# Kernel optimization log

Measured on AMD Instinct MI355X. Metric: run time of the kernel, lower is better.

## Reference

```python
import jax, jax.numpy as jnp
import numpy as np

N_NODES = 100000
N_EDGES = 3200000
F_IN = 16
F_HID = 32


def _gcn_conv(x, row, col, edge_w, W, b, num_nodes):
    # PyG GCNConv: gcn_norm with add_self_loops=True (fill_value=1.0),
    # symmetric normalization, then x @ W.T aggregated over edges, + bias.
    loop = jnp.arange(num_nodes)
    r = jnp.concatenate([row, loop])
    c = jnp.concatenate([col, loop])
    ew = jnp.concatenate([edge_w, jnp.ones((num_nodes,), dtype=edge_w.dtype)])
    deg = jax.ops.segment_sum(ew, c, num_segments=num_nodes)
    dis = jnp.where(deg > 0, jax.lax.rsqrt(deg), 0.0)
    norm = dis[r] * ew * dis[c]  # [E+N]
    xw = x @ W.T                 # [N, out]
    msg = xw[r] * norm[:, None]  # gather + scale
    out = jax.ops.segment_sum(msg, c, num_segments=num_nodes)
    return out + b


def setup_inputs() -> dict:
    key = jax.random.key(0)
    ks = jax.random.split(key, 8)
    x = jax.random.normal(ks[0], (N_NODES, F_IN), dtype=jnp.float32)
    edge_index = jax.random.randint(ks[1], (2, N_EDGES), 0, N_NODES, dtype=jnp.int64)
    edge_w = jax.random.uniform(ks[2], (N_EDGES,), dtype=jnp.float32)
    W1 = jax.random.normal(ks[3], (F_HID, F_IN), dtype=jnp.float32) * 0.1
    b1 = jax.random.normal(ks[4], (F_HID,), dtype=jnp.float32) * 0.1
    W2 = jax.random.normal(ks[5], (F_IN, F_HID), dtype=jnp.float32) * 0.1
    b2 = jax.random.normal(ks[6], (F_IN,), dtype=jnp.float32) * 0.1
    return {"x": x, "edge_index": edge_index, "edge_w": edge_w,
            "W1": W1, "b1": b1, "W2": W2, "b2": b2, "num_nodes": N_NODES}


def reference(x, edge_index, edge_w, W1, b1, W2, b2, num_nodes):
    row, col = edge_index[0], edge_index[1]
    h = _gcn_conv(x, row, col, edge_w, W1, b1, num_nodes)
    h = jax.nn.relu(h)
    out = _gcn_conv(h, row, col, edge_w, W2, b2, num_nodes)
    return out
```

## Files before the change

### kernel.cpp

```cpp
#include <hip/hip_runtime.h>
#include <hip/hip_fp16.h>
#include <cstdint>


#define BS 256
#define CHUNKS 256
#define NST 1024

__device__ __forceinline__ int2 nt_load_edge(const int2* p) {
    long long v = __builtin_nontemporal_load((const long long*)p);
    int2 r;
    r.x = (int)(v & 0xFFFFFFFFll);
    r.y = (int)(v >> 32);
    return r;
}

__device__ __forceinline__ float4 load_h4(const __half* p) {
    uint2 u = *(const uint2*)p;
    __half2 p0 = *(__half2*)&u.x;
    __half2 p1 = *(__half2*)&u.y;
    float2 f0 = __half22float2(p0);
    float2 f1 = __half22float2(p1);
    float4 r;
    r.x = f0.x; r.y = f0.y; r.z = f1.x; r.w = f1.y;
    return r;
}

__global__ __launch_bounds__(1024) void hist_kernel(
        const int* __restrict__ col, int* __restrict__ part,
        int E, int nbuck, int per) {
    extern __shared__ int sh[];
    for (int t = threadIdx.x; t < nbuck; t += blockDim.x) sh[t] = 0;
    __syncthreads();
    int lo = blockIdx.x * per, hi = min(E, lo + per);
    for (int e = lo + threadIdx.x; e < hi; e += blockDim.x)
        atomicAdd(&sh[col[e] >> 8], 1);
    __syncthreads();
    for (int t = threadIdx.x; t < nbuck; t += blockDim.x)
        part[(size_t)blockIdx.x * nbuck + t] = sh[t];
}

__global__ void colscan_kernel(const int* __restrict__ part, int* __restrict__ base,
                               int* __restrict__ tot, int nbuck) {
    int b = blockIdx.x;
    if (b >= nbuck) return;
    int lane = threadIdx.x;
    int off = 0;
    for (int g = 0; g < CHUNKS; g += 64) {
        int c = g + lane;
        int v = part[(size_t)c * nbuck + b];
        int s = v;
        #pragma unroll
        for (int d = 1; d < 64; d <<= 1) {
            int t = __shfl_up(s, d);
            if (lane >= d) s += t;
        }
        base[(size_t)c * nbuck + b] = off + (s - v);
        off += __shfl(s, 63);
    }
    if (lane == 0) tot[b] = off;
}

__global__ void bscan_kernel(const int* __restrict__ tot, int* __restrict__ start,
                             int nbuck, int E) {
    __shared__ int s[512];
    int tid = threadIdx.x;
    int v = (tid < nbuck) ? tot[tid] : 0;
    s[tid] = v;
    __syncthreads();
    for (int off = 1; off < 512; off <<= 1) {
        int t = (tid >= off) ? s[tid - off] : 0;
        __syncthreads();
        s[tid] += t;
        __syncthreads();
    }
    if (tid < nbuck) start[tid] = s[tid] - v;
    if (tid == 0) start[nbuck] = E;
}

__global__ __launch_bounds__(1024) void place_kernel(
        const int* __restrict__ row, const int* __restrict__ col,
        const float* __restrict__ ew,
        const int* __restrict__ start, const int* __restrict__ base,
        int2* __restrict__ rw, int E, int nbuck, int per) {
    extern __shared__ int sh[];
    int* lbase = sh;
    int* cnt2  = sh + nbuck;
    int c = blockIdx.x;
    for (int t = threadIdx.x; t < nbuck; t += blockDim.x) {
        lbase[t] = start[t] + base[(size_t)c * nbuck + t];
        cnt2[t] = 0;
    }
    __syncthreads();
    int lo = c * per, hi = min(E, lo + per);
    const int stride = blockDim.x;
    int e = lo + threadIdx.x;
    for (; e + 3 * stride < hi; e += 4 * stride) {
        int cc[4], rr[4];
        float w[4];
#pragma unroll
        for (int k = 0; k < 4; ++k) {
            cc[k] = col[e + k * stride];
            rr[k] = row[e + k * stride];
            w[k]  = ew[e + k * stride];
        }
        int p[4];
#pragma unroll
        for (int k = 0; k < 4; ++k) {
            int b = cc[k] >> 8;
            p[k] = lbase[b] + atomicAdd(&cnt2[b], 1);
        }
#pragma unroll
        for (int k = 0; k < 4; ++k) {
            int2 v;
            v.x = rr[k] | ((cc[k] & 255) << 20);
            v.y = __float_as_int(w[k]);
            rw[p[k]] = v;
        }
    }
    for (; e < hi; e += stride) {
        int cc = col[e];
        int b = cc >> 8;
        int p = lbase[b] + atomicAdd(&cnt2[b], 1);
        int2 v;
        v.x = row[e] | ((cc & 255) << 20);
        v.y = __float_as_int(ew[e]);
        rw[p] = v;
    }
}

__global__ __launch_bounds__(NST) void nodesort_kernel(
        const int2* __restrict__ rw, const int* __restrict__ start,
        int2* __restrict__ rw2, int* __restrict__ ptr,
        float* __restrict__ dis, int N, int E, int nbuck) {
    __shared__ int cnt[BS];
    __shared__ float fdeg[BS];
    __shared__ int fill[BS];
    __shared__ int stmp[BS];
    int b = blockIdx.x, tid = threadIdx.x;
    if (tid < BS) { cnt[tid] = 0; fdeg[tid] = 0.f; }
    __syncthreads();
    int s0 = start[b], s1 = start[b + 1];

    {
        int e = s0 + tid;
        for (; e + 3 * NST < s1; e += 4 * NST) {
            int2 v[4];
#pragma unroll
            for (int k = 0; k < 4; ++k) v[k] = rw[e + k * NST];
#pragma unroll
            for (int k = 0; k < 4; ++k) {
                int cl = v[k].x >> 20;
                atomicAdd(&cnt[cl], 1);
                atomicAdd(&fdeg[cl], __int_as_float(v[k].y));
            }
        }
        for (; e < s1; e += NST) {
            int2 v = rw[e];
            int cl = v.x >> 20;
            atomicAdd(&cnt[cl], 1);
            atomicAdd(&fdeg[cl], __int_as_float(v.y));
        }
    }
    __syncthreads();

    int myc = 0;
    if (tid < BS) { myc = cnt[tid]; stmp[tid] = myc; }
    __syncthreads();
    for (int off = 1; off < BS; off <<= 1) {
        int t = 0;
        if (tid < BS && tid >= off) t = stmp[tid - off];
        __syncthreads();
        if (tid < BS) stmp[tid] += t;
        __syncthreads();
    }
    if (tid < BS) {
        int excl = stmp[tid] - myc;
        ptr[b * BS + tid] = s0 + excl;
        fill[tid] = excl;
        int node = b * BS + tid;
        if (node < N) dis[node] = rsqrtf(fdeg[tid] + 1.0f);
    }
    __syncthreads();

    {
        int e = s0 + tid;
        for (; e + 3 * NST < s1; e += 4 * NST) {
            int2 v[4];
#pragma unroll
            for (int k = 0; k < 4; ++k) v[k] = rw[e + k * NST];
            int p[4];
#pragma unroll
            for (int k = 0; k < 4; ++k)
                p[k] = s0 + atomicAdd(&fill[v[k].x >> 20], 1);
#pragma unroll
            for (int k = 0; k < 4; ++k) {
                int2 o;
                o.x = (v[k].x & 0xFFFFF) << 5;
                o.y = v[k].y;
                rw2[p[k]] = o;
            }
        }
        for (; e < s1; e += NST) {
            int2 v = rw[e];
            int p = s0 + atomicAdd(&fill[v.x >> 20], 1);
            int2 o;
            o.x = (v.x & 0xFFFFF) << 5;
            o.y = v.y;
            rw2[p] = o;
        }
    }
    if (b == 0 && tid == 0) ptr[nbuck * BS] = E;
}

__global__ void xsc_kernel(const float* __restrict__ x, const float* __restrict__ dis,
                           __half* __restrict__ xsc, int N) {
    int i = blockIdx.x * 256 + threadIdx.x;
    if (i >= N) return;
    float d = dis[i];
    const float4* xr = (const float4*)(x + (size_t)i * 16);
    __half2 h[8];
#pragma unroll
    for (int k = 0; k < 4; ++k) {
        float4 v = xr[k];
        h[2*k]   = __floats2half2_rn(v.x * d, v.y * d);
        h[2*k+1] = __floats2half2_rn(v.z * d, v.w * d);
    }
    uint4* dst = (uint4*)(xsc + (size_t)i * 16);
    dst[0] = *(uint4*)&h[0];
    dst[1] = *(uint4*)&h[4];
}

template <int FINAL>
__global__ __launch_bounds__(256) void gather_kernel(
        const int* __restrict__ ptr, const int2* __restrict__ rw2,
        const __half* __restrict__ src, const float* __restrict__ dis,
        const float* __restrict__ b2, float* __restrict__ dst, int N) {
    int tid  = threadIdx.x;
    int wave = tid >> 6;
    int lane = tid & 63;
    int g = lane >> 4;
    int s = (lane >> 2) & 3;
    int q = lane & 3;
    int node = (blockIdx.x * 4 + wave) * 4 + g;
    if (node >= N) return;
    int s0 = ptr[node], s1 = ptr[node + 1];

    const char* srcb = (const char*)src;
    float4 a0 = {0.f, 0.f, 0.f, 0.f}, a1 = {0.f, 0.f, 0.f, 0.f};
    int e = s0 + s;
    for (; e + 4 < s1; e += 8) {
        int2 v0 = nt_load_edge(&rw2[e]);
        int2 v1 = nt_load_edge(&rw2[e + 4]);
        float4 x0 = load_h4((const __half*)(srcb + v0.x) + q * 4);
        float4 x1 = load_h4((const __half*)(srcb + v1.x) + q * 4);
        float w0 = __int_as_float(v0.y), w1 = __int_as_float(v1.y);
        a0.x += w0 * x0.x; a0.y += w0 * x0.y; a0.z += w0 * x0.z; a0.w += w0 * x0.w;
        a1.x += w1 * x1.x; a1.y += w1 * x1.y; a1.z += w1 * x1.z; a1.w += w1 * x1.w;
    }
    if (e < s1) {
        int2 v0 = nt_load_edge(&rw2[e]);
        float4 x0 = load_h4((const __half*)(srcb + v0.x) + q * 4);
        float w0 = __int_as_float(v0.y);
        a0.x += w0 * x0.x; a0.y += w0 * x0.y; a0.z += w0 * x0.z; a0.w += w0 * x0.w;
    }
    a0.x += a1.x; a0.y += a1.y; a0.z += a1.z; a0.w += a1.w;
#pragma unroll
    for (int m = 4; m <= 8; m <<= 1) {
        a0.x += __shfl_xor(a0.x, m);
        a0.y += __shfl_xor(a0.y, m);
        a0.z += __shfl_xor(a0.z, m);
        a0.w += __shfl_xor(a0.w, m);
    }

    if (s == 0) {
        float d = dis[node];
        float4 self = load_h4((const __half*)(srcb + ((size_t)node << 5)) + q * 4);
        float4 o;
        o.x = d * (a0.x + self.x);
        o.y = d * (a0.y + self.y);
        o.z = d * (a0.z + self.z);
        o.w = d * (a0.w + self.w);
        if (FINAL) {
            float4 bb = *(const float4*)(b2 + q * 4);
            o.x += bb.x; o.y += bb.y; o.z += bb.z; o.w += bb.w;
        }
        *(float4*)(dst + (size_t)node * 16 + q * 4) = o;
    }
}

__global__ __launch_bounds__(256) void mlp_kernel(
        const float* __restrict__ t, const float* __restrict__ dis,
        const float* __restrict__ W1, const float* __restrict__ b1,
        const float* __restrict__ W2, __half* __restrict__ xs2, int N) {
    __shared__ float sW1[512];
    __shared__ float sW2[512];
    __shared__ float sb1[32];
    for (int k = threadIdx.x; k < 512; k += 256) {
        sW1[k] = W1[k];
        sW2[k] = W2[k];
    }
    if (threadIdx.x < 32) sb1[threadIdx.x] = b1[threadIdx.x];
    __syncthreads();
    int i = blockIdx.x * 256 + threadIdx.x;
    if (i >= N) return;

    float tr[16];
#pragma unroll
    for (int k = 0; k < 4; ++k) {
        float4 v = ((const float4*)(t + (size_t)i * 16))[k];
        tr[4*k+0] = v.x; tr[4*k+1] = v.y; tr[4*k+2] = v.z; tr[4*k+3] = v.w;
    }
    float h[32];
#pragma unroll
    for (int o = 0; o < 32; ++o) {
        float acc = sb1[o];
#pragma unroll
        for (int k = 0; k < 16; ++k) acc += tr[k] * sW1[o * 16 + k];
        h[o] = fmaxf(acc, 0.f);
    }
    float d = dis[i];
    float o16[16];
#pragma unroll
    for (int o = 0; o < 16; ++o) {
        float acc = 0.f;
#pragma unroll
        for (int k = 0; k < 32; ++k) acc += h[k] * sW2[o * 32 + k];
        o16[o] = acc * d;
    }
    __half2 hh[8];
#pragma unroll
    for (int k = 0; k < 8; ++k) hh[k] = __floats2half2_rn(o16[2*k], o16[2*k+1]);
    uint4* dst = (uint4*)(xs2 + (size_t)i * 16);
    dst[0] = *(uint4*)&hh[0];
    dst[1] = *(uint4*)&hh[4];
}

extern "C" void kernel_launch(void* const* d_in, const int* in_sizes, int n_in,
                              void* d_out, int out_size, void* d_ws, size_t ws_size,
                              hipStream_t stream) {
    const float* x  = (const float*)d_in[0];
    const int*   ei = (const int*)d_in[1];
    const float* ew = (const float*)d_in[2];
    const float* W1 = (const float*)d_in[3];
    const float* b1 = (const float*)d_in[4];
    const float* W2 = (const float*)d_in[5];
    const float* b2 = (const float*)d_in[6];
    float* out = (float*)d_out;

    const int N = in_sizes[0] / 16;
    const int E = in_sizes[2];
    const int* row = ei;
    const int* col = ei + E;

    const int nbuck = (N + BS - 1) / BS;
    const int per   = (E + CHUNKS - 1) / CHUNKS;

    float*  ws    = (float*)d_ws;
    int2*   rw2   = (int2*)ws;
    int2*   rw    = (int2*)(ws + (size_t)2 * E);
    __half* xsc   = (__half*)(ws + (size_t)2 * E);
    float*  tbuf  = ws + (size_t)2 * E + (size_t)8 * N;
    __half* xs2   = (__half*)(ws + (size_t)2 * E + (size_t)24 * N);
    float*  dis   = ws + (size_t)4 * E;
    int*    ptr   = (int*)(dis + N);
    int*    part  = ptr + (size_t)BS * nbuck + 1;
    int*    base  = part + (size_t)CHUNKS * nbuck;
    int*    tot   = base + (size_t)CHUNKS * nbuck;
    int*    start = tot + nbuck;

    hist_kernel<<<CHUNKS, 1024, nbuck * 4, stream>>>(col, part, E, nbuck, per);
    colscan_kernel<<<nbuck, 64, 0, stream>>>(part, base, tot, nbuck);
    bscan_kernel<<<1, 512, 0, stream>>>(tot, start, nbuck, E);
    place_kernel<<<CHUNKS, 1024, 2 * nbuck * 4, stream>>>(row, col, ew, start, base, rw, E, nbuck, per);
    nodesort_kernel<<<nbuck, NST, 0, stream>>>(rw, start, rw2, ptr, dis, N, E, nbuck);

    xsc_kernel<<<(N + 255) / 256, 256, 0, stream>>>(x, dis, xsc, N);
    {
        int gblocks = (N + 15) / 16;
        gather_kernel<0><<<gblocks, 256, 0, stream>>>(ptr, rw2, xsc, dis, b2, tbuf, N);
        mlp_kernel<<<(N + 255) / 256, 256, 0, stream>>>(tbuf, dis, W1, b1, W2, xs2, N);
        gather_kernel<1><<<gblocks, 256, 0, stream>>>(ptr, rw2, xs2, dis, b2, out, N);
    }
}
```

Baseline: 175.1 us.

## Pack count and fixed-point degree into one atomic, fuse x scaling into nodesort

The per-node edge count and weighted degree are packed into a single 64-bit shared-memory atomic, using the high bits for the count and 24-bit fixed point for the weight. This halves the shared atomics in the histogram pass. The separate xsc kernel is folded into nodesort, so each bucket block scales its 256 nodes' features by dis and writes fp16, removing one launch. Because the xsc buffer used to alias the rw region that nodesort still reads, it gets a new workspace location. The fixed-point degree adds quantisation error and can overflow if a node's summed weight exceeds 2^16.

```diff
diff --git a/kernel.cpp b/kernel.cpp
--- a/kernel.cpp
+++ b/kernel.cpp
@@ -131,14 +131,16 @@
 
 __global__ __launch_bounds__(NST) void nodesort_kernel(
         const int2* __restrict__ rw, const int* __restrict__ start,
+        const float* __restrict__ x,
         int2* __restrict__ rw2, int* __restrict__ ptr,
-        float* __restrict__ dis, int N, int E, int nbuck) {
-    __shared__ int cnt[BS];
-    __shared__ float fdeg[BS];
+        float* __restrict__ dis, __half* __restrict__ xsc,
+        int N, int E, int nbuck) {
+    __shared__ unsigned long long cd[BS];
     __shared__ int fill[BS];
     __shared__ int stmp[BS];
+    __shared__ float sdis[BS];
     int b = blockIdx.x, tid = threadIdx.x;
-    if (tid < BS) { cnt[tid] = 0; fdeg[tid] = 0.f; }
+    if (tid < BS) cd[tid] = 0ull;
     __syncthreads();
     int s0 = start[b], s1 = start[b + 1];
 
@@ -151,21 +153,25 @@
 #pragma unroll
             for (int k = 0; k < 4; ++k) {
                 int cl = v[k].x >> 20;
-                atomicAdd(&cnt[cl], 1);
-                atomicAdd(&fdeg[cl], __int_as_float(v[k].y));
+                float w = __int_as_float(v[k].y);
+                unsigned long long enc =
+                    (1ull << 40) | (unsigned long long)(w * 16777216.0f);
+                atomicAdd(&cd[cl], enc);
             }
         }
         for (; e < s1; e += NST) {
             int2 v = rw[e];
             int cl = v.x >> 20;
-            atomicAdd(&cnt[cl], 1);
-            atomicAdd(&fdeg[cl], __int_as_float(v.y));
+            float w = __int_as_float(v.y);
+            unsigned long long enc =
+                (1ull << 40) | (unsigned long long)(w * 16777216.0f);
+            atomicAdd(&cd[cl], enc);
         }
     }
     __syncthreads();
 
     int myc = 0;
-    if (tid < BS) { myc = cnt[tid]; stmp[tid] = myc; }
+    if (tid < BS) { myc = (int)(cd[tid] >> 40); stmp[tid] = myc; }
     __syncthreads();
     for (int off = 1; off < BS; off <<= 1) {
         int t = 0;
@@ -178,10 +184,28 @@
         int excl = stmp[tid] - myc;
         ptr[b * BS + tid] = s0 + excl;
         fill[tid] = excl;
+        float deg = (float)(cd[tid] & ((1ull << 40) - 1)) * (1.0f / 16777216.0f);
+        float d = rsqrtf(deg + 1.0f);
+        sdis[tid] = d;
         int node = b * BS + tid;
-        if (node < N) dis[node] = rsqrtf(fdeg[tid] + 1.0f);
-    }
-    __syncthreads();
+        if (node < N) dis[node] = d;
+    }
+    __syncthreads();
+
+    {
+        int nl = tid >> 2, quad = tid & 3;
+        int node = b * BS + nl;
+        if (node < N) {
+            float d = sdis[nl];
+            float4 v = *(const float4*)(x + (size_t)node * 16 + quad * 4);
+            __half2 h0 = __floats2half2_rn(v.x * d, v.y * d);
+            __half2 h1 = __floats2half2_rn(v.z * d, v.w * d);
+            uint2 u;
+            u.x = *(unsigned int*)&h0;
+            u.y = *(unsigned int*)&h1;
+            *(uint2*)(xsc + (size_t)node * 16 + quad * 4) = u;
+        }
+    }
 
     {
         int e = s0 + tid;
@@ -211,24 +235,6 @@
         }
     }
     if (b == 0 && tid == 0) ptr[nbuck * BS] = E;
-}
-
-__global__ void xsc_kernel(const float* __restrict__ x, const float* __restrict__ dis,
-                           __half* __restrict__ xsc, int N) {
-    int i = blockIdx.x * 256 + threadIdx.x;
-    if (i >= N) return;
-    float d = dis[i];
-    const float4* xr = (const float4*)(x + (size_t)i * 16);
-    __half2 h[8];
-#pragma unroll
-    for (int k = 0; k < 4; ++k) {
-        float4 v = xr[k];
-        h[2*k]   = __floats2half2_rn(v.x * d, v.y * d);
-        h[2*k+1] = __floats2half2_rn(v.z * d, v.w * d);
-    }
-    uint4* dst = (uint4*)(xsc + (size_t)i * 16);
-    dst[0] = *(uint4*)&h[0];
-    dst[1] = *(uint4*)&h[4];
 }
 
 template <int FINAL>
@@ -359,23 +365,22 @@
     float*  ws    = (float*)d_ws;
     int2*   rw2   = (int2*)ws;
     int2*   rw    = (int2*)(ws + (size_t)2 * E);
-    __half* xsc   = (__half*)(ws + (size_t)2 * E);
-    float*  tbuf  = ws + (size_t)2 * E + (size_t)8 * N;
-    __half* xs2   = (__half*)(ws + (size_t)2 * E + (size_t)24 * N);
+    float*  tbuf  = ws + (size_t)2 * E;
+    __half* xs2   = (__half*)(ws + (size_t)2 * E + (size_t)16 * N);
     float*  dis   = ws + (size_t)4 * E;
     int*    ptr   = (int*)(dis + N);
     int*    part  = ptr + (size_t)BS * nbuck + 1;
     int*    base  = part + (size_t)CHUNKS * nbuck;
     int*    tot   = base + (size_t)CHUNKS * nbuck;
     int*    start = tot + nbuck;
+    __half* xsc   = (__half*)(start + nbuck + 1);
 
     hist_kernel<<<CHUNKS, 1024, nbuck * 4, stream>>>(col, part, E, nbuck, per);
     colscan_kernel<<<nbuck, 64, 0, stream>>>(part, base, tot, nbuck);
     bscan_kernel<<<1, 512, 0, stream>>>(tot, start, nbuck, E);
     place_kernel<<<CHUNKS, 1024, 2 * nbuck * 4, stream>>>(row, col, ew, start, base, rw, E, nbuck, per);
-    nodesort_kernel<<<nbuck, NST, 0, stream>>>(rw, start, rw2, ptr, dis, N, E, nbuck);
-
-    xsc_kernel<<<(N + 255) / 256, 256, 0, stream>>>(x, dis, xsc, N);
+    nodesort_kernel<<<nbuck, NST, 0, stream>>>(rw, start, x, rw2, ptr, dis, xsc, N, E, nbuck);
+
     {
         int gblocks = (N + 15) / 16;
         gather_kernel<0><<<gblocks, 256, 0, stream>>>(ptr, rw2, xsc, dis, b2, tbuf, N);
```

Result: faster. 162.4 us (-7.2%).
